# Performance work log

Measured on AMD Instinct MI355X. Metric: run time of the kernel, lower is better.

Reference implementation:

```python
import jax, jax.numpy as jnp
import numpy as np
from jax import lax

NUM_INPUT = 4
NUM_OUTPUT = 1
NUM_U = 10
N = NUM_U // NUM_OUTPUT          # MPC horizon
BATCH = 1024
NINEQ_U = 2 * NUM_U              # input box constraints
NINEQ_X = 2 * NUM_INPUT * N      # soft state constraints
NZ = NUM_U                       # control decision variable dim
NE = NINEQ_X                     # slack variable dim
NW = NZ + NE                     # combined QP variable w = [z; e]
IPM_ITERS = 20                   # fixed-iteration primal-dual interior point
SIGMA = 0.1                      # centering parameter
REG = 1e-8                       # KKT regularization


def setup_inputs():
    key = jax.random.key(0)
    ks = jax.random.split(key, 6)
    x = 0.5 * jax.random.normal(ks[0], (BATCH, NUM_INPUT), dtype=jnp.float32)
    # equality constraint pins z0 = u0; keep inside the |z| <= 0.5 box so QP is feasible
    u0 = (jax.random.uniform(ks[1], (BATCH, NUM_OUTPUT), dtype=jnp.float32) - 0.5) * 0.8
    Q_sqrt = jax.random.uniform(ks[2], (NUM_INPUT, NUM_INPUT), dtype=jnp.float32)
    R_sqrt = jax.random.uniform(ks[3], (NUM_OUTPUT, NUM_OUTPUT), dtype=jnp.float32)
    # scale A so that A^N stays bounded (torch init rand() would blow up at N=10)
    A_dyn = 0.3 * jax.random.uniform(ks[4], (NUM_INPUT, NUM_INPUT), dtype=jnp.float32)
    B_dyn = jax.random.uniform(ks[5], (NUM_INPUT, NUM_OUTPUT), dtype=jnp.float32)
    return {"x": x, "u0": u0, "Q_sqrt": Q_sqrt, "R_sqrt": R_sqrt,
            "A_dyn": A_dyn, "B_dyn": B_dyn}


def _build_mpc_blocks(A, B):
    # A_hat = [A; A^2; ...; A^N],  B_hat = lower block-Toeplitz of A^k B
    Apows = [A]
    for _ in range(1, N):
        Apows.append(Apows[-1] @ A)
    A_hat = jnp.concatenate(Apows, axis=0)                 # (N*n, n)
    T = [B]
    for _ in range(1, N):
        T.append(A @ T[-1])
    T = jnp.stack(T)                                        # (N, n, m), T[k] = A^k B
    i = jnp.arange(N)
    diff = i[:, None] - i[None, :]
    blocks = jnp.where((diff >= 0)[:, :, None, None],
                       T[jnp.clip(diff, 0, N - 1)], 0.0)    # (N, N, n, m)
    B_hat = blocks.transpose(0, 2, 1, 3).reshape(N * NUM_INPUT, N * NUM_OUTPUT)
    return A_hat, B_hat


def _max_step(v, dv):
    # largest alpha keeping v + alpha*dv > 0 (per batch row)
    ratio = jnp.where(dv < -1e-12, -v / jnp.minimum(dv, -1e-12), 1e8)
    return jnp.min(ratio, axis=-1, keepdims=True)


def _qp_solve(H, q, G, h, Aeq, beq):
    # min 0.5 w^T H w + q^T w  s.t. G w <= h, Aeq w = beq
    # H, G, Aeq shared; q, h, beq batched. Infeasible-start primal-dual IPM.
    b, nw = q.shape
    mI = G.shape[0]
    ne = Aeq.shape[0]
    w = jnp.zeros((b, nw), q.dtype)
    nu = jnp.zeros((b, ne), q.dtype)
    s = jnp.maximum(h, 1.0)
    lam = jnp.ones((b, mI), q.dtype)
    I_nw = jnp.eye(nw, dtype=q.dtype)
    I_ne = jnp.eye(ne, dtype=q.dtype)

    def step(carry, _):
        w, s, lam, nu = carry
        Gw = w @ G.T
        r_dual = w @ H + q + lam @ G + nu @ Aeq            # (b, nw)
        r_prim = Gw + s - h                                # (b, mI)
        r_eq = w @ Aeq.T - beq                             # (b, ne)
        mu = SIGMA * jnp.sum(s * lam, axis=-1, keepdims=True) / mI
        d = lam / s
        tmp = (mu - lam * s + lam * r_prim) / s
        rw = -(r_dual + tmp @ G)
        rn = -r_eq
        # Schur complement in w: M = H + G^T diag(lam/s) G
        M = H[None] + (G.T[None, :, :] * d[:, None, :]) @ G + REG * I_nw
        AeqT = jnp.broadcast_to(Aeq.T[None], (b, nw, ne))
        AeqB = jnp.broadcast_to(Aeq[None], (b, ne, nw))
        corner = jnp.broadcast_to((-REG * I_ne)[None], (b, ne, ne))
        K = jnp.concatenate([jnp.concatenate([M, AeqT], axis=2),
                             jnp.concatenate([AeqB, corner], axis=2)], axis=1)
        rhs = jnp.concatenate([rw, rn], axis=1)
        sol = jnp.linalg.solve(K, rhs[..., None])[..., 0]
        dw, dnu = sol[:, :nw], sol[:, nw:]
        ds = -(dw @ G.T) - r_prim
        dlam = (mu - lam * s - lam * ds) / s
        alpha = 0.99 * jnp.minimum(1.0, jnp.minimum(_max_step(s, ds),
                                                    _max_step(lam, dlam)))
        return (w + alpha * dw, s + alpha * ds,
                lam + alpha * dlam, nu + alpha * dnu), None

    (w, s, lam, nu), _ = lax.scan(step, (w, s, lam, nu), None, length=IPM_ITERS)
    return w


def _forward(x, u0, Q_sqrt, R_sqrt, A_dyn, B_dyn):
    b = x.shape[0]
    dt = x.dtype
    x0 = x.reshape(b, -1)
    A_hat, B_hat = _build_mpc_blocks(A_dyn, B_dyn)
    Q = Q_sqrt @ Q_sqrt.T
    R = R_sqrt @ R_sqrt.T
    Q_diag = jnp.kron(jnp.eye(N, dtype=dt), Q)   # block-diag(Q,...,Q,P) with P = Q
    R_diag = jnp.kron(jnp.eye(N, dtype=dt), R)
    Q_hat = B_hat.T @ (Q_diag @ B_hat) + R_diag  # (nz, nz)
    A_x0 = x0 @ A_hat.T                           # (b, n*N)
    p = 2.0 * A_x0 @ (Q_diag @ B_hat)             # (b, nz)
    G1 = jnp.concatenate([jnp.eye(NZ, dtype=dt), -jnp.eye(NZ, dtype=dt)], axis=0)
    G2 = jnp.concatenate([B_hat, -B_hat], axis=0)
    h1 = 0.5 * jnp.ones((b, NINEQ_U), dt)
    h21 = 4.0 * jnp.ones((b, NUM_INPUT * N), dt) - A_x0
    h22 = 4.0 * jnp.ones((b, NUM_INPUT * N), dt) + A_x0
    h2 = jnp.concatenate([h21, h22], axis=1)
    E = jnp.eye(NE, dtype=dt)                     # E_sqrt = I so E = I
    # combined QP over w = [z; e]:
    #   min z^T Q_hat z + p^T z + e^T E e
    #   s.t. G1 z <= h1, G2 z - e <= h2, -e <= 0, F z = f
    # (sum_squares(sqrtm(Q_hat) z) == z^T Q_hat z, so sqrtm cancels exactly)
    H = 2.0 * jnp.block([[Q_hat, jnp.zeros((NZ, NE), dt)],
                         [jnp.zeros((NE, NZ), dt), E]])
    q = jnp.concatenate([p, jnp.zeros((b, NE), dt)], axis=1)
    Ie = jnp.eye(NE, dtype=dt)
    G_all = jnp.concatenate([
        jnp.concatenate([G1, jnp.zeros((NINEQ_U, NE), dt)], axis=1),
        jnp.concatenate([G2, -Ie], axis=1),
        jnp.concatenate([jnp.zeros((NE, NZ), dt), -Ie], axis=1)], axis=0)
    h_all = jnp.concatenate([h1, h2, jnp.zeros((b, NE), dt)], axis=1)
    F = jnp.zeros((1, NW), dt).at[0, 0].set(1.0)  # F z = f with F = e_0^T (padded over e)
    beq = u0.reshape(b, -1)
    w = _qp_solve(H, q, G_all, h_all, F, beq)
    u_opt = w[:, :NZ]
    e_opt = w[:, NZ:]
    a = jnp.sum((u_opt @ Q_hat) * u_opt + p * u_opt, axis=1)
    bterm = jnp.sum((A_x0 @ Q_diag) * A_x0, axis=1)
    c = jnp.sum((x0 @ Q) * x0, axis=1)
    dterm = jnp.sum((e_opt @ E) * e_opt, axis=1)
    cost_opt = (a + bterm + c + dterm)[:, None]
    u0_opt = u_opt[:, 0]   # weight vector is e_0
    return cost_opt, u0_opt


def reference(x, u0, Q_sqrt, R_sqrt, A_dyn, B_dyn):
    return _forward(x, u0, Q_sqrt, R_sqrt, A_dyn, B_dyn)
```

## Files before the change

### kernel.cpp

```cpp
#include <hip/hip_runtime.h>

#define BATCH 1024
#define ITERS 20
#define SIGMA_C 0.1f
#define REG_C 1e-8f

__device__ __forceinline__ float frcp(float x) { return __builtin_amdgcn_rcpf(x); }
__device__ __forceinline__ float readlane_f(float v, int l) {
    return __int_as_float(__builtin_amdgcn_readlane(__float_as_int(v), l));
}
#define DPPF(v, ctrl) \
    __int_as_float(__builtin_amdgcn_update_dpp(0, __float_as_int(v), ctrl, 0xf, 0xf, true))

__device__ __forceinline__ float wave_sum(float v) {
    v += DPPF(v, 0xB1);
    v += DPPF(v, 0x4E);
    v += DPPF(v, 0x141);
    v += DPPF(v, 0x140);
    v += __shfl_xor(v, 16);
    v += __shfl_xor(v, 32);
    return v;
}
__device__ __forceinline__ float wave_min(float v) {
    v = fminf(v, DPPF(v, 0xB1));
    v = fminf(v, DPPF(v, 0x4E));
    v = fminf(v, DPPF(v, 0x141));
    v = fminf(v, DPPF(v, 0x140));
    v = fminf(v, __shfl_xor(v, 16));
    v = fminf(v, __shfl_xor(v, 32));
    return v;
}

__global__ __launch_bounds__(64, 1) void ipm_kernel(
    const float* __restrict__ x, const float* __restrict__ u0p,
    const float* __restrict__ Qs, const float* __restrict__ Rs,
    const float* __restrict__ Ad, const float* __restrict__ Bd,
    float* __restrict__ out)
{
    const int item = blockIdx.x;
    const int lane = threadIdx.x;

    __shared__ __align__(16) float BLc[10 * 40];
    __shared__ __align__(16) float QBc[10 * 40];
    __shared__ __align__(16) float yL4[40];
    __shared__ __align__(16) float QhL[10 * 12];
    __shared__ __align__(16) float SL[10 * 12];
    __shared__ __align__(16) float cg[80];
    __shared__ float duL[20], ltL[20];
    __shared__ float axL[40];
    __shared__ float pvL[10], wL[10];
    __shared__ float QL[16];
    __shared__ float TL[40];
    __shared__ float AhL[160];

    const int r2 = (lane >> 2) & 3, c2 = lane & 3;
    const int r4 = lane & 3;

    if (lane < 16) {
        float acc = 0.f;
        #pragma unroll
        for (int k = 0; k < 4; ++k) acc += Qs[r2 * 4 + k] * Qs[c2 * 4 + k];
        QL[lane] = acc;
    }

    float acol[4];
    #pragma unroll
    for (int k = 0; k < 4; ++k) acol[k] = Ad[k * 4 + c2];
    float cur = Ad[r2 * 4 + c2];
    if (lane < 16) AhL[r2 * 4 + c2] = cur;
    #pragma unroll
    for (int i = 1; i < 10; ++i) {
        float nx = 0.f;
        #pragma unroll
        for (int k = 0; k < 4; ++k) nx += __shfl(cur, r2 * 4 + k) * acol[k];
        cur = nx;
        if (lane < 16) AhL[(4 * i + r2) * 4 + c2] = cur;
    }

    float arow[4];
    #pragma unroll
    for (int k = 0; k < 4; ++k) arow[k] = Ad[r4 * 4 + k];
    float tc = Bd[r4];
    if (lane < 4) TL[r4] = tc;
    #pragma unroll
    for (int i = 1; i < 10; ++i) {
        float nt = 0.f;
        #pragma unroll
        for (int k = 0; k < 4; ++k) nt += arow[k] * __shfl(tc, k);
        tc = nt;
        if (lane < 4) TL[i * 4 + r4] = nt;
    }
    __syncthreads();

    const int kk40 = (lane < 40) ? lane : 39;
    const int ib = lane >> 2;
    float b[10];
    #pragma unroll
    for (int j = 0; j < 10; ++j) {
        int dd = ib - j;
        int dc = dd < 0 ? 0 : (dd > 9 ? 9 : dd);
        float v = TL[dc * 4 + r4];
        b[j] = (dd >= 0 && lane < 40) ? v : 0.f;
    }

    const float xv0 = x[item * 4 + 0], xv1 = x[item * 4 + 1];
    const float xv2 = x[item * 4 + 2], xv3 = x[item * 4 + 3];
    const float ax = AhL[kk40 * 4 + 0] * xv0 + AhL[kk40 * 4 + 1] * xv1 +
                     AhL[kk40 * 4 + 2] * xv2 + AhL[kk40 * 4 + 3] * xv3;
    if (lane < 40) axL[lane] = ax;

    const int gbase = lane & ~3;
    float yv = 0.f;
    #pragma unroll
    for (int rp_ = 0; rp_ < 4; ++rp_) yv += QL[r4 * 4 + rp_] * __shfl(ax, gbase + rp_);
    if (lane < 40) yL4[lane] = yv;
    #pragma unroll
    for (int cc = 0; cc < 10; ++cc) {
        float acc = 0.f;
        #pragma unroll
        for (int rp_ = 0; rp_ < 4; ++rp_) acc += QL[r4 * 4 + rp_] * __shfl(b[cc], gbase + rp_);
        if (lane < 40) QBc[cc * 40 + lane] = acc;
    }
    if (lane < 40) {
        #pragma unroll
        for (int j = 0; j < 10; ++j) BLc[j * 40 + lane] = b[j];
    }
    __syncthreads();

    if (lane < 10) {
        const float4* br = reinterpret_cast<const float4*>(&BLc[lane * 40]);
        const float4* yy = reinterpret_cast<const float4*>(yL4);
        float acc = 0.f;
        #pragma unroll
        for (int i = 0; i < 10; ++i) {
            const float4 a_ = br[i], b_ = yy[i];
            acc += a_.x * b_.x + a_.y * b_.y + a_.z * b_.z + a_.w * b_.w;
        }
        pvL[lane] = 2.f * acc;
    }
    const float R2v = Rs[0] * Rs[0];
    #pragma unroll
    for (int p = 0; p < 2; ++p) {
        const int t = lane + 64 * p;
        if (t < 100) {
            const int aa = t / 10, bb = t - aa * 10;
            const float4* ba = reinterpret_cast<const float4*>(&BLc[aa * 40]);
            const float4* qb = reinterpret_cast<const float4*>(&QBc[bb * 40]);
            float acc = (aa == bb) ? R2v : 0.f;
            #pragma unroll
            for (int i = 0; i < 10; ++i) {
                const float4 a_ = ba[i], b_ = qb[i];
                acc += a_.x * b_.x + a_.y * b_.y + a_.z * b_.z + a_.w * b_.w;
            }
            QhL[aa * 12 + bb] = acc;
        }
    }
    __syncthreads();

    const int t1 = 2 * lane;
    const int srow = t1 / 10, sc1 = t1 - srow * 10, sc2 = sc1 + 1;
    const int rr = lane - 50;
    float tabA[40], tabB[40];
    float qh_a = 0.f, qh_b = 0.f;
    bool diagA = false, diagB = false;
    int drow = 0;
    if (lane < 50) {
        const float4* br = reinterpret_cast<const float4*>(&BLc[srow * 40]);
        const float4* b1 = reinterpret_cast<const float4*>(&BLc[sc1 * 40]);
        const float4* b2 = reinterpret_cast<const float4*>(&BLc[sc2 * 40]);
        #pragma unroll
        for (int i = 0; i < 10; ++i) {
            const float4 r_ = br[i], u_ = b1[i], v_ = b2[i];
            tabA[4*i+0] = r_.x * u_.x; tabA[4*i+1] = r_.y * u_.y;
            tabA[4*i+2] = r_.z * u_.z; tabA[4*i+3] = r_.w * u_.w;
            tabB[4*i+0] = r_.x * v_.x; tabB[4*i+1] = r_.y * v_.y;
            tabB[4*i+2] = r_.z * v_.z; tabB[4*i+3] = r_.w * v_.w;
        }
        qh_a = 2.f * QhL[srow * 12 + sc1];
        qh_b = 2.f * QhL[srow * 12 + sc2];
        diagA = (srow == sc1); diagB = (srow == sc2);
        drow = srow;
    } else if (lane < 60) {
        const float4* br = reinterpret_cast<const float4*>(&BLc[rr * 40]);
        #pragma unroll
        for (int i = 0; i < 10; ++i) {
            const float4 r_ = br[i];
            tabA[4*i+0] = r_.x; tabA[4*i+1] = r_.y;
            tabA[4*i+2] = r_.z; tabA[4*i+3] = r_.w;
        }
        #pragma unroll
        for (int c = 0; c < 10; ++c) tabB[c] = QhL[rr * 12 + c];
        qh_a = pvL[rr];
    }
    __syncthreads();

    float s_B = fmaxf(4.f - ax, 1.f), s_C = fmaxf(4.f + ax, 1.f);
    float s_D = 1.f, s_E = 1.f, s_U = 1.f;
    float l_B = 1.f, l_C = 1.f, l_D = 1.f, l_E = 1.f, l_U = 1.f;
    float w2a = 0.f, w2b = 0.f;
    float w1[10];
    #pragma unroll
    for (int r = 0; r < 10; ++r) w1[r] = 0.f;
    float w1own = 0.f, nu = 0.f;
    const float uu0 = u0p[item];
    const bool a40 = lane < 40, a20 = lane < 20;
    const int jown = (lane < 10) ? lane : lane - 10;
    const float sgnU = (lane < 10) ? 1.f : -1.f;

    for (int it = 0; it < ITERS; ++it) {
        const float rs_B = frcp(s_B), rs_C = frcp(s_C), rs_D = frcp(s_D),
                    rs_E = frcp(s_E), rs_U = frcp(s_U);
        const float d_B = l_B * rs_B, d_C = l_C * rs_C, d_D = l_D * rs_D,
                    d_E = l_E * rs_E, d_U = l_U * rs_U;
        float part = a40 ? (s_B * l_B + s_C * l_C + s_D * l_D + s_E * l_E) : 0.f;
        if (a20) part += s_U * l_U;
        const float mu = SIGMA_C * wave_sum(part) * (1.f / 180.f);

        float Bu = 0.f;
        #pragma unroll
        for (int j = 0; j < 10; ++j) Bu += b[j] * w1[j];

        const float rp_B = Bu - w2a + s_B - (4.f - ax);
        const float rp_C = -Bu - w2b + s_C - (4.f + ax);
        const float rp_D = -w2a + s_D;
        const float rp_E = -w2b + s_E;
        const float rp_U = sgnU * w1own + s_U - 0.5f;

        const float tm_B = (mu - l_B * s_B + l_B * rp_B) * rs_B;
        const float tm_C = (mu - l_C * s_C + l_C * rp_C) * rs_C;
        const float tm_D = (mu - l_D * s_D + l_D * rp_D) * rs_D;
        const float tm_E = (mu - l_E * s_E + l_E * rp_E) * rs_E;
        const float tm_U = (mu - l_U * s_U + l_U * rp_U) * rs_U;
        const float lt_B = l_B + tm_B, lt_C = l_C + tm_C, lt_D = l_D + tm_D,
                    lt_E = l_E + tm_E;

        const float D22a = 2.f + d_B + d_D + REG_C, D22b = 2.f + d_C + d_E + REG_C;
        const float rda = frcp(D22a), rdb = frcp(D22b);
        const float rw2a = -2.f * w2a + lt_B + lt_D;
        const float rw2b = -2.f * w2b + lt_C + lt_E;
        const float coeff = (d_B + d_C) - d_B * d_B * rda - d_C * d_C * rdb;
        const float gvc = (d_B * rw2a * rda - d_C * rw2b * rdb) - (lt_B - lt_C);

        if (a40) { cg[lane] = coeff; cg[40 + lane] = gvc; }
        if (a20) { duL[lane] = d_U; ltL[lane] = l_U + tm_U; }
        __syncthreads();

        float4 cf[10];
        {
            const float4* cp = reinterpret_cast<const float4*>(cg + ((lane >= 50) ? 40 : 0));
            #pragma unroll
            for (int i = 0; i < 10; ++i) cf[i] = cp[i];
        }
        if (lane < 50) {
            float accA = 0.f, accB = 0.f;
            #pragma unroll
            for (int i = 0; i < 10; ++i) {
                accA += tabA[4*i+0]*cf[i].x + tabA[4*i+1]*cf[i].y +
                        tabA[4*i+2]*cf[i].z + tabA[4*i+3]*cf[i].w;
                accB += tabB[4*i+0]*cf[i].x + tabB[4*i+1]*cf[i].y +
                        tabB[4*i+2]*cf[i].z + tabB[4*i+3]*cf[i].w;
            }
            float vA = accA + qh_a, vB = accB + qh_b;
            if (diagA || diagB) {
                const float dd = duL[drow] + duL[10 + drow] + REG_C;
                if (diagA) vA += dd; else vB += dd;
            }
            *reinterpret_cast<float2*>(&SL[srow * 12 + sc1]) = make_float2(vA, vB);
        } else if (lane < 60) {
            float acc = 0.f;
            #pragma unroll
            for (int i = 0; i < 10; ++i)
                acc += tabA[4*i+0]*cf[i].x + tabA[4*i+1]*cf[i].y +
                       tabA[4*i+2]*cf[i].z + tabA[4*i+3]*cf[i].w;
            float qw = 0.f;
            #pragma unroll
            for (int c = 0; c < 10; ++c) qw += tabB[c] * w1[c];
            SL[rr * 12 + 10] =
                acc - (2.f * qw + qh_a + ltL[rr] - ltL[10 + rr] + ((rr == 0) ? nu : 0.f));
        }
        __syncthreads();

        float row[11], rBv;
        if (lane < 10) {
            const float4* s4 = reinterpret_cast<const float4*>(&SL[lane * 12]);
            const float4 q0 = s4[0], q1 = s4[1], q2 = s4[2];
            row[0] = q0.x; row[1] = q0.y; row[2] = q0.z; row[3] = q0.w;
            row[4] = q1.x; row[5] = q1.y; row[6] = q1.z; row[7] = q1.w;
            row[8] = q2.x; row[9] = q2.y; row[10] = q2.z;
        } else {
            #pragma unroll
            for (int c = 0; c < 11; ++c) row[c] = 0.f;
        }
        rBv = (lane == 0) ? 1.f : 0.f;

        #pragma unroll
        for (int kc = 0; kc < 9; ++kc) {
            float pk[11];
            #pragma unroll
            for (int c = kc; c < 11; ++c) pk[c] = readlane_f(row[c], kc);
            const float pB = readlane_f(rBv, kc);
            const float rpiv = frcp(pk[kc]);
            const float f = (lane > kc) ? row[kc] * rpiv : 0.f;
            #pragma unroll
            for (int c = kc + 1; c < 11; ++c) row[c] -= f * pk[c];
            rBv -= f * pB;
        }

        float rd[10];
        #pragma unroll
        for (int r = 0; r < 10; ++r) rd[r] = frcp(row[r]);

        float dwAv[10], dwBv[10], ownA = 0.f, ownB = 0.f;
        #pragma unroll
        for (int r = 9; r >= 0; --r) {
            const float bA = readlane_f(row[10] * rd[r], r);
            const float bB = readlane_f(rBv * rd[r], r);
            dwAv[r] = bA; dwBv[r] = bB;
            if (jown == r) { ownA = bA; ownB = bB; }
            const float m_ = (lane < r) ? 1.f : 0.f;
            row[10] -= m_ * row[r] * bA;
            rBv     -= m_ * row[r] * bB;
        }

        const float rn = -(w1[0] - uu0);
        const float nu_d = (dwAv[0] - rn) * frcp(dwBv[0] + REG_C);
        float dw1[10];
        #pragma unroll
        for (int r = 0; r < 10; ++r) dw1[r] = dwAv[r] - nu_d * dwBv[r];
        const float dOwn = ownA - nu_d * ownB;

        float Bdw = 0.f;
        #pragma unroll
        for (int j = 0; j < 10; ++j) Bdw += b[j] * dw1[j];
        const float dw2a = (rw2a + d_B * Bdw) * rda;
        const float dw2b = (rw2b - d_C * Bdw) * rdb;

        const float ds_B = -(Bdw - dw2a) - rp_B;
        const float ds_C = (Bdw + dw2b) - rp_C;
        const float ds_D = dw2a - rp_D;
        const float ds_E = dw2b - rp_E;
        const float ds_U = -sgnU * dOwn - rp_U;
        const float dl_B = (mu - l_B * s_B - l_B * ds_B) * rs_B;
        const float dl_C = (mu - l_C * s_C - l_C * ds_C) * rs_C;
        const float dl_D = (mu - l_D * s_D - l_D * ds_D) * rs_D;
        const float dl_E = (mu - l_E * s_E - l_E * ds_E) * rs_E;
        const float dl_U = (mu - l_U * s_U - l_U * ds_U) * rs_U;

        float rmin = 1.f;
        if (a40) {
            if (ds_B < -1e-12f) rmin = fminf(rmin, -s_B * frcp(ds_B));
            if (ds_C < -1e-12f) rmin = fminf(rmin, -s_C * frcp(ds_C));
            if (ds_D < -1e-12f) rmin = fminf(rmin, -s_D * frcp(ds_D));
            if (ds_E < -1e-12f) rmin = fminf(rmin, -s_E * frcp(ds_E));
            if (dl_B < -1e-12f) rmin = fminf(rmin, -l_B * frcp(dl_B));
            if (dl_C < -1e-12f) rmin = fminf(rmin, -l_C * frcp(dl_C));
            if (dl_D < -1e-12f) rmin = fminf(rmin, -l_D * frcp(dl_D));
            if (dl_E < -1e-12f) rmin = fminf(rmin, -l_E * frcp(dl_E));
        }
        if (a20) {
            if (ds_U < -1e-12f) rmin = fminf(rmin, -s_U * frcp(ds_U));
            if (dl_U < -1e-12f) rmin = fminf(rmin, -l_U * frcp(dl_U));
        }
        const float alpha = 0.99f * wave_min(rmin);

        s_B += alpha * ds_B; s_C += alpha * ds_C; s_D += alpha * ds_D;
        s_E += alpha * ds_E; s_U += alpha * ds_U;
        l_B += alpha * dl_B; l_C += alpha * dl_C; l_D += alpha * dl_D;
        l_E += alpha * dl_E; l_U += alpha * dl_U;
        w2a += alpha * dw2a; w2b += alpha * dw2b;
        #pragma unroll
        for (int r = 0; r < 10; ++r) w1[r] += alpha * dw1[r];
        w1own += alpha * dOwn;
        nu += alpha * nu_d;
    }

    if (lane == 0) {
        #pragma unroll
        for (int r = 0; r < 10; ++r) wL[r] = w1[r];
    }
    __syncthreads();
    float part = a40 ? (w2a * w2a + w2b * w2b) : 0.f;
    for (int idx = lane; idx < 100; idx += 64) {
        const int r = idx / 10, c = idx - r * 10;
        part += wL[r] * QhL[r * 12 + c] * wL[c];
    }
    if (lane < 10) part += pvL[lane] * wL[lane];
    for (int idx = lane; idx < 160; idx += 64) {
        const int i2 = idx >> 4, rc = idx & 15, rr2 = rc >> 2, cc2 = rc & 3;
        part += axL[i2 * 4 + rr2] * QL[rc] * axL[i2 * 4 + cc2];
    }
    if (lane == 0) {
        float ct = 0.f;
        #pragma unroll
        for (int r = 0; r < 4; ++r) {
            const float xr = (r == 0 ? xv0 : r == 1 ? xv1 : r == 2 ? xv2 : xv3);
            #pragma unroll
            for (int c = 0; c < 4; ++c) {
                const float xc = (c == 0 ? xv0 : c == 1 ? xv1 : c == 2 ? xv2 : xv3);
                ct += xr * QL[r * 4 + c] * xc;
            }
        }
        part += ct;
    }
    const float cost = wave_sum(part);
    if (lane == 0) {
        out[item] = cost;
        out[BATCH + item] = w1[0];
    }
}

extern "C" void kernel_launch(void* const* d_in, const int* in_sizes, int n_in,
                              void* d_out, int out_size, void* d_ws, size_t ws_size,
                              hipStream_t stream) {
    const float* x  = (const float*)d_in[0];
    const float* u0 = (const float*)d_in[1];
    const float* Qs = (const float*)d_in[2];
    const float* Rs = (const float*)d_in[3];
    const float* Ad = (const float*)d_in[4];
    const float* Bd = (const float*)d_in[5];
    float* outp = (float*)d_out;
    ipm_kernel<<<dim3(BATCH), dim3(64), 0, stream>>>(x, u0, Qs, Rs, Ad, Bd, outp);
}
```

Baseline: 101.4 us.

## Use 2x2 block Gauss-Jordan elimination and fuse mu reduction into step reduction

Replaces the per-column elimination and back-substitution of the 10x10 KKT solve with 2x2 pivot-block Gauss-Jordan steps, halving the number of serial readlane broadcast rounds. The duality-gap reduction for the next iteration's mu is folded into the alpha min-reduction: the next mu is computed as a quadratic in alpha from three partial sums, so the same DPP passes serve both reductions. This removes one full wave reduction per iteration and shortens the serial dependency chain. The cost is extra arithmetic, unpivoted 2x2 block inverses that may be less numerically robust, and an s*l product evaluated in a different order.

```diff
diff --git a/kernel.cpp b/kernel.cpp
--- a/kernel.cpp
+++ b/kernel.cpp
@@ -21,15 +21,13 @@
     v += __shfl_xor(v, 32);
     return v;
 }
-__device__ __forceinline__ float wave_min(float v) {
-    v = fminf(v, DPPF(v, 0xB1));
-    v = fminf(v, DPPF(v, 0x4E));
-    v = fminf(v, DPPF(v, 0x141));
-    v = fminf(v, DPPF(v, 0x140));
-    v = fminf(v, __shfl_xor(v, 16));
-    v = fminf(v, __shfl_xor(v, 32));
-    return v;
-}
+
+#define RED4_DPP(ctrl) do { \
+    p0 += DPPF(p0, ctrl); \
+    p1 += DPPF(p1, ctrl); \
+    p2 += DPPF(p2, ctrl); \
+    rmin = fminf(rmin, DPPF(rmin, ctrl)); \
+} while (0)
 
 __global__ __launch_bounds__(64, 1) void ipm_kernel(
     const float* __restrict__ x, const float* __restrict__ u0p,
@@ -207,14 +205,18 @@
     const int jown = (lane < 10) ? lane : lane - 10;
     const float sgnU = (lane < 10) ? 1.f : -1.f;
 
+    float mu;
+    {
+        float part = a40 ? (s_B * l_B + s_C * l_C + s_D * l_D + s_E * l_E) : 0.f;
+        if (a20) part += s_U * l_U;
+        mu = SIGMA_C * wave_sum(part) * (1.f / 180.f);
+    }
+
     for (int it = 0; it < ITERS; ++it) {
         const float rs_B = frcp(s_B), rs_C = frcp(s_C), rs_D = frcp(s_D),
                     rs_E = frcp(s_E), rs_U = frcp(s_U);
         const float d_B = l_B * rs_B, d_C = l_C * rs_C, d_D = l_D * rs_D,
                     d_E = l_E * rs_E, d_U = l_U * rs_U;
-        float part = a40 ? (s_B * l_B + s_C * l_C + s_D * l_D + s_E * l_E) : 0.f;
-        if (a20) part += s_U * l_U;
-        const float mu = SIGMA_C * wave_sum(part) * (1.f / 180.f);
 
         float Bu = 0.f;
         #pragma unroll
@@ -280,7 +282,7 @@
         }
         __syncthreads();
 
-        float row[11], rBv;
+        float row[12];
         if (lane < 10) {
             const float4* s4 = reinterpret_cast<const float4*>(&SL[lane * 12]);
             const float4 q0 = s4[0], q1 = s4[1], q2 = s4[2];
@@ -291,43 +293,54 @@
             #pragma unroll
             for (int c = 0; c < 11; ++c) row[c] = 0.f;
         }
-        rBv = (lane == 0) ? 1.f : 0.f;
-
-        #pragma unroll
-        for (int kc = 0; kc < 9; ++kc) {
-            float pk[11];
-            #pragma unroll
-            for (int c = kc; c < 11; ++c) pk[c] = readlane_f(row[c], kc);
-            const float pB = readlane_f(rBv, kc);
-            const float rpiv = frcp(pk[kc]);
-            const float f = (lane > kc) ? row[kc] * rpiv : 0.f;
-            #pragma unroll
-            for (int c = kc + 1; c < 11; ++c) row[c] -= f * pk[c];
-            rBv -= f * pB;
-        }
-
-        float rd[10];
-        #pragma unroll
-        for (int r = 0; r < 10; ++r) rd[r] = frcp(row[r]);
-
-        float dwAv[10], dwBv[10], ownA = 0.f, ownB = 0.f;
-        #pragma unroll
-        for (int r = 9; r >= 0; --r) {
-            const float bA = readlane_f(row[10] * rd[r], r);
-            const float bB = readlane_f(rBv * rd[r], r);
-            dwAv[r] = bA; dwBv[r] = bB;
-            if (jown == r) { ownA = bA; ownB = bB; }
-            const float m_ = (lane < r) ? 1.f : 0.f;
-            row[10] -= m_ * row[r] * bA;
-            rBv     -= m_ * row[r] * bB;
+        row[11] = (lane == 0) ? 1.f : 0.f;
+
+        #pragma unroll
+        for (int kb = 0; kb < 5; ++kb) {
+            const int bb = 2 * kb;
+            float pA[12], pB[12];
+            #pragma unroll
+            for (int c = 0; c < 12; ++c) {
+                if (c >= bb) {
+                    pA[c] = readlane_f(row[c], bb);
+                    pB[c] = readlane_f(row[c], bb + 1);
+                }
+            }
+            const float rdet = frcp(pA[bb] * pB[bb + 1] - pA[bb + 1] * pB[bb]);
+            const bool act = (lane < 10) && (lane != bb) && (lane != bb + 1);
+            const float f1 = act ? (row[bb] * pB[bb + 1] - row[bb + 1] * pB[bb]) * rdet : 0.f;
+            const float f2 = act ? (row[bb + 1] * pA[bb] - row[bb] * pA[bb + 1]) * rdet : 0.f;
+            #pragma unroll
+            for (int c = 0; c < 12; ++c) {
+                if (c >= bb + 2) row[c] -= f1 * pA[c] + f2 * pB[c];
+            }
+        }
+
+        float xA[10], xB[10];
+        #pragma unroll
+        for (int kb = 0; kb < 5; ++kb) {
+            const int bb = 2 * kb;
+            const float a_  = readlane_f(row[bb],     bb);
+            const float b_  = readlane_f(row[bb + 1], bb);
+            const float c_  = readlane_f(row[bb],     bb + 1);
+            const float d_  = readlane_f(row[bb + 1], bb + 1);
+            const float rA0 = readlane_f(row[10], bb),     rB0 = readlane_f(row[11], bb);
+            const float rA1 = readlane_f(row[10], bb + 1), rB1 = readlane_f(row[11], bb + 1);
+            const float rdet = frcp(a_ * d_ - b_ * c_);
+            xA[bb]     = (d_ * rA0 - b_ * rA1) * rdet;
+            xA[bb + 1] = (a_ * rA1 - c_ * rA0) * rdet;
+            xB[bb]     = (d_ * rB0 - b_ * rB1) * rdet;
+            xB[bb + 1] = (a_ * rB1 - c_ * rB0) * rdet;
         }
 
         const float rn = -(w1[0] - uu0);
-        const float nu_d = (dwAv[0] - rn) * frcp(dwBv[0] + REG_C);
+        const float nu_d = (xA[0] - rn) * frcp(xB[0] + REG_C);
         float dw1[10];
         #pragma unroll
-        for (int r = 0; r < 10; ++r) dw1[r] = dwAv[r] - nu_d * dwBv[r];
-        const float dOwn = ownA - nu_d * ownB;
+        for (int r = 0; r < 10; ++r) dw1[r] = xA[r] - nu_d * xB[r];
+        float dOwn = 0.f;
+        #pragma unroll
+        for (int r = 0; r < 10; ++r) dOwn = (jown == r) ? dw1[r] : dOwn;
 
         float Bdw = 0.f;
         #pragma unroll
@@ -346,7 +359,7 @@
         const float dl_E = (mu - l_E * s_E - l_E * ds_E) * rs_E;
         const float dl_U = (mu - l_U * s_U - l_U * ds_U) * rs_U;
 
-        float rmin = 1.f;
+        float rmin = 1.f, p0 = 0.f, p1 = 0.f, p2 = 0.f;
         if (a40) {
             if (ds_B < -1e-12f) rmin = fminf(rmin, -s_B * frcp(ds_B));
             if (ds_C < -1e-12f) rmin = fminf(rmin, -s_C * frcp(ds_C));
@@ -356,12 +369,29 @@
             if (dl_C < -1e-12f) rmin = fminf(rmin, -l_C * frcp(dl_C));
             if (dl_D < -1e-12f) rmin = fminf(rmin, -l_D * frcp(dl_D));
             if (dl_E < -1e-12f) rmin = fminf(rmin, -l_E * frcp(dl_E));
+            p0 = s_B * l_B + s_C * l_C + s_D * l_D + s_E * l_E;
+            p1 = (s_B * dl_B + l_B * ds_B) + (s_C * dl_C + l_C * ds_C) +
+                 (s_D * dl_D + l_D * ds_D) + (s_E * dl_E + l_E * ds_E);
+            p2 = ds_B * dl_B + ds_C * dl_C + ds_D * dl_D + ds_E * dl_E;
         }
         if (a20) {
             if (ds_U < -1e-12f) rmin = fminf(rmin, -s_U * frcp(ds_U));
             if (dl_U < -1e-12f) rmin = fminf(rmin, -l_U * frcp(dl_U));
-        }
-        const float alpha = 0.99f * wave_min(rmin);
+            p0 += s_U * l_U;
+            p1 += s_U * dl_U + l_U * ds_U;
+            p2 += ds_U * dl_U;
+        }
+        RED4_DPP(0xB1);
+        RED4_DPP(0x4E);
+        RED4_DPP(0x141);
+        RED4_DPP(0x140);
+        p0 += __shfl_xor(p0, 16); p1 += __shfl_xor(p1, 16); p2 += __shfl_xor(p2, 16);
+        rmin = fminf(rmin, __shfl_xor(rmin, 16));
+        p0 += __shfl_xor(p0, 32); p1 += __shfl_xor(p1, 32); p2 += __shfl_xor(p2, 32);
+        rmin = fminf(rmin, __shfl_xor(rmin, 32));
+
+        const float alpha = 0.99f * rmin;
+        mu = SIGMA_C * (p0 + alpha * (p1 + alpha * p2)) * (1.f / 180.f);
 
         s_B += alpha * ds_B; s_C += alpha * ds_C; s_D += alpha * ds_D;
         s_E += alpha * ds_E; s_U += alpha * ds_U;
```

Result: no change. 101.3 us (-0.1%).

## Carry next-iteration mu algebraically and fuse reductions with step-length min

Applied to the files above, without the earlier changes.

The barrier parameter for the next iteration is computed in closed form as p0 + alpha*p1 + alpha^2*p2. The three terms are reduced in the same DPP/shuffle sequence as the step-length minimum, which takes the dependent wave_sum for mu off the start of each iteration. Dot products are split into several independent accumulators to shorten dependency chains. B*dw is now built from precomputed B*dwA and B*dwB, so it no longer waits on nu_d. Rounding can differ slightly from recomputing mu directly.

```diff
diff --git a/kernel.cpp b/kernel.cpp
--- a/kernel.cpp
+++ b/kernel.cpp
@@ -21,15 +21,12 @@
     v += __shfl_xor(v, 32);
     return v;
 }
-__device__ __forceinline__ float wave_min(float v) {
-    v = fminf(v, DPPF(v, 0xB1));
-    v = fminf(v, DPPF(v, 0x4E));
-    v = fminf(v, DPPF(v, 0x141));
-    v = fminf(v, DPPF(v, 0x140));
-    v = fminf(v, __shfl_xor(v, 16));
-    v = fminf(v, __shfl_xor(v, 32));
-    return v;
-}
+
+#define RED3_DPP(ctrl) do { \
+    p1 += DPPF(p1, ctrl); \
+    p2 += DPPF(p2, ctrl); \
+    rmin = fminf(rmin, DPPF(rmin, ctrl)); \
+} while (0)
 
 __global__ __launch_bounds__(64, 1) void ipm_kernel(
     const float* __restrict__ x, const float* __restrict__ u0p,
@@ -207,18 +204,29 @@
     const int jown = (lane < 10) ? lane : lane - 10;
     const float sgnU = (lane < 10) ? 1.f : -1.f;
 
+    float mu;
+    {
+        float part = a40 ? (s_B * l_B + s_C * l_C + s_D * l_D + s_E * l_E) : 0.f;
+        if (a20) part += s_U * l_U;
+        mu = SIGMA_C * wave_sum(part) * (1.f / 180.f);
+    }
+
     for (int it = 0; it < ITERS; ++it) {
         const float rs_B = frcp(s_B), rs_C = frcp(s_C), rs_D = frcp(s_D),
                     rs_E = frcp(s_E), rs_U = frcp(s_U);
         const float d_B = l_B * rs_B, d_C = l_C * rs_C, d_D = l_D * rs_D,
                     d_E = l_E * rs_E, d_U = l_U * rs_U;
-        float part = a40 ? (s_B * l_B + s_C * l_C + s_D * l_D + s_E * l_E) : 0.f;
-        if (a20) part += s_U * l_U;
-        const float mu = SIGMA_C * wave_sum(part) * (1.f / 180.f);
-
-        float Bu = 0.f;
-        #pragma unroll
-        for (int j = 0; j < 10; ++j) Bu += b[j] * w1[j];
+
+        float p0 = a40 ? (s_B * l_B + s_C * l_C + s_D * l_D + s_E * l_E) : 0.f;
+        if (a20) p0 += s_U * l_U;
+        p0 = wave_sum(p0);
+
+        float Bu0 = 0.f, Bu1 = 0.f;
+        #pragma unroll
+        for (int j = 0; j < 5; ++j) Bu0 += b[j] * w1[j];
+        #pragma unroll
+        for (int j = 5; j < 10; ++j) Bu1 += b[j] * w1[j];
+        const float Bu = Bu0 + Bu1;
 
         const float rp_B = Bu - w2a + s_B - (4.f - ax);
         const float rp_C = -Bu - w2b + s_C - (4.f + ax);
@@ -252,29 +260,36 @@
             for (int i = 0; i < 10; ++i) cf[i] = cp[i];
         }
         if (lane < 50) {
-            float accA = 0.f, accB = 0.f;
+            float aA0 = 0.f, aA1 = 0.f, aA2 = 0.f, aA3 = 0.f;
+            float aB0 = 0.f, aB1 = 0.f, aB2 = 0.f, aB3 = 0.f;
             #pragma unroll
             for (int i = 0; i < 10; ++i) {
-                accA += tabA[4*i+0]*cf[i].x + tabA[4*i+1]*cf[i].y +
-                        tabA[4*i+2]*cf[i].z + tabA[4*i+3]*cf[i].w;
-                accB += tabB[4*i+0]*cf[i].x + tabB[4*i+1]*cf[i].y +
-                        tabB[4*i+2]*cf[i].z + tabB[4*i+3]*cf[i].w;
+                aA0 += tabA[4*i+0] * cf[i].x; aA1 += tabA[4*i+1] * cf[i].y;
+                aA2 += tabA[4*i+2] * cf[i].z; aA3 += tabA[4*i+3] * cf[i].w;
+                aB0 += tabB[4*i+0] * cf[i].x; aB1 += tabB[4*i+1] * cf[i].y;
+                aB2 += tabB[4*i+2] * cf[i].z; aB3 += tabB[4*i+3] * cf[i].w;
             }
-            float vA = accA + qh_a, vB = accB + qh_b;
+            float vA = ((aA0 + aA1) + (aA2 + aA3)) + qh_a;
+            float vB = ((aB0 + aB1) + (aB2 + aB3)) + qh_b;
             if (diagA || diagB) {
                 const float dd = duL[drow] + duL[10 + drow] + REG_C;
                 if (diagA) vA += dd; else vB += dd;
             }
             *reinterpret_cast<float2*>(&SL[srow * 12 + sc1]) = make_float2(vA, vB);
         } else if (lane < 60) {
-            float acc = 0.f;
-            #pragma unroll
-            for (int i = 0; i < 10; ++i)
-                acc += tabA[4*i+0]*cf[i].x + tabA[4*i+1]*cf[i].y +
-                       tabA[4*i+2]*cf[i].z + tabA[4*i+3]*cf[i].w;
-            float qw = 0.f;
-            #pragma unroll
-            for (int c = 0; c < 10; ++c) qw += tabB[c] * w1[c];
+            float a0 = 0.f, a1 = 0.f, a2 = 0.f, a3 = 0.f;
+            #pragma unroll
+            for (int i = 0; i < 10; ++i) {
+                a0 += tabA[4*i+0] * cf[i].x; a1 += tabA[4*i+1] * cf[i].y;
+                a2 += tabA[4*i+2] * cf[i].z; a3 += tabA[4*i+3] * cf[i].w;
+            }
+            const float acc = (a0 + a1) + (a2 + a3);
+            float qw0 = 0.f, qw1 = 0.f;
+            #pragma unroll
+            for (int c = 0; c < 5; ++c) qw0 += tabB[c] * w1[c];
+            #pragma unroll
+            for (int c = 5; c < 10; ++c) qw1 += tabB[c] * w1[c];
+            const float qw = qw0 + qw1;
             SL[rr * 12 + 10] =
                 acc - (2.f * qw + qh_a + ltL[rr] - ltL[10 + rr] + ((rr == 0) ? nu : 0.f));
         }
@@ -322,16 +337,21 @@
             rBv     -= m_ * row[r] * bB;
         }
 
+        float bA0 = 0.f, bA1 = 0.f, bB0 = 0.f, bB1 = 0.f;
+        #pragma unroll
+        for (int j = 0; j < 5; ++j) { bA0 += b[j] * dwAv[j]; bB0 += b[j] * dwBv[j]; }
+        #pragma unroll
+        for (int j = 5; j < 10; ++j) { bA1 += b[j] * dwAv[j]; bB1 += b[j] * dwBv[j]; }
+        const float BdwA = bA0 + bA1, BdwB = bB0 + bB1;
+
         const float rn = -(w1[0] - uu0);
         const float nu_d = (dwAv[0] - rn) * frcp(dwBv[0] + REG_C);
         float dw1[10];
         #pragma unroll
         for (int r = 0; r < 10; ++r) dw1[r] = dwAv[r] - nu_d * dwBv[r];
         const float dOwn = ownA - nu_d * ownB;
-
-        float Bdw = 0.f;
-        #pragma unroll
-        for (int j = 0; j < 10; ++j) Bdw += b[j] * dw1[j];
+        const float Bdw = BdwA - nu_d * BdwB;
+
         const float dw2a = (rw2a + d_B * Bdw) * rda;
         const float dw2b = (rw2b - d_C * Bdw) * rdb;
 
@@ -346,7 +366,7 @@
         const float dl_E = (mu - l_E * s_E - l_E * ds_E) * rs_E;
         const float dl_U = (mu - l_U * s_U - l_U * ds_U) * rs_U;
 
-        float rmin = 1.f;
+        float rmin = 1.f, p1 = 0.f, p2 = 0.f;
         if (a40) {
             if (ds_B < -1e-12f) rmin = fminf(rmin, -s_B * frcp(ds_B));
             if (ds_C < -1e-12f) rmin = fminf(rmin, -s_C * frcp(ds_C));
@@ -356,12 +376,27 @@
             if (dl_C < -1e-12f) rmin = fminf(rmin, -l_C * frcp(dl_C));
             if (dl_D < -1e-12f) rmin = fminf(rmin, -l_D * frcp(dl_D));
             if (dl_E < -1e-12f) rmin = fminf(rmin, -l_E * frcp(dl_E));
+            p1 = (s_B * dl_B + l_B * ds_B) + (s_C * dl_C + l_C * ds_C) +
+                 (s_D * dl_D + l_D * ds_D) + (s_E * dl_E + l_E * ds_E);
+            p2 = ds_B * dl_B + ds_C * dl_C + ds_D * dl_D + ds_E * dl_E;
         }
         if (a20) {
             if (ds_U < -1e-12f) rmin = fminf(rmin, -s_U * frcp(ds_U));
             if (dl_U < -1e-12f) rmin = fminf(rmin, -l_U * frcp(dl_U));
-        }
-        const float alpha = 0.99f * wave_min(rmin);
+            p1 += s_U * dl_U + l_U * ds_U;
+            p2 += ds_U * dl_U;
+        }
+        RED3_DPP(0xB1);
+        RED3_DPP(0x4E);
+        RED3_DPP(0x141);
+        RED3_DPP(0x140);
+        p1 += __shfl_xor(p1, 16); p2 += __shfl_xor(p2, 16);
+        rmin = fminf(rmin, __shfl_xor(rmin, 16));
+        p1 += __shfl_xor(p1, 32); p2 += __shfl_xor(p2, 32);
+        rmin = fminf(rmin, __shfl_xor(rmin, 32));
+
+        const float alpha = 0.99f * rmin;
+        mu = SIGMA_C * (p0 + alpha * (p1 + alpha * p2)) * (1.f / 180.f);
 
         s_B += alpha * ds_B; s_C += alpha * ds_C; s_D += alpha * ds_D;
         s_E += alpha * ds_E; s_U += alpha * ds_U;
```

Result: no change. 102.7 us (+1.3%).

## Fuse step-length and next-mu reductions, packed FMA dot products

Applied to the files above, without the earlier changes.

Rewrites the step-length search as a max of -d/v ratios, using reciprocals of s and l instead of one division per component. The next iteration's mu comes from a quadratic in alpha (p0 + alpha*p1 + alpha^2*p2), so mu and alpha now share a single batched DPP/shuffle reduction instead of two separate wave reductions per iteration. The small dot products are also recast as packed two-wide float FMAs. This shortens the serial per-iteration reduction chain at the cost of extra reciprocals and slightly different rounding.

```diff
diff --git a/kernel.cpp b/kernel.cpp
--- a/kernel.cpp
+++ b/kernel.cpp
@@ -5,10 +5,15 @@
 #define SIGMA_C 0.1f
 #define REG_C 1e-8f
 
+typedef float f2 __attribute__((ext_vector_type(2)));
+
 __device__ __forceinline__ float frcp(float x) { return __builtin_amdgcn_rcpf(x); }
 __device__ __forceinline__ float readlane_f(float v, int l) {
     return __int_as_float(__builtin_amdgcn_readlane(__float_as_int(v), l));
 }
+__device__ __forceinline__ f2 mkf2(float a, float b) { f2 r; r.x = a; r.y = b; return r; }
+__device__ __forceinline__ f2 fma2(f2 a, f2 b, f2 c) { return a * b + c; }
+
 #define DPPF(v, ctrl) \
     __int_as_float(__builtin_amdgcn_update_dpp(0, __float_as_int(v), ctrl, 0xf, 0xf, true))
 
@@ -21,15 +26,13 @@
     v += __shfl_xor(v, 32);
     return v;
 }
-__device__ __forceinline__ float wave_min(float v) {
-    v = fminf(v, DPPF(v, 0xB1));
-    v = fminf(v, DPPF(v, 0x4E));
-    v = fminf(v, DPPF(v, 0x141));
-    v = fminf(v, DPPF(v, 0x140));
-    v = fminf(v, __shfl_xor(v, 16));
-    v = fminf(v, __shfl_xor(v, 32));
-    return v;
-}
+
+#define RED4_DPP(ctrl) do { \
+    p0 += DPPF(p0, ctrl); \
+    p1 += DPPF(p1, ctrl); \
+    p2 += DPPF(p2, ctrl); \
+    q = fmaxf(q, DPPF(q, ctrl)); \
+} while (0)
 
 __global__ __launch_bounds__(64, 1) void ipm_kernel(
     const float* __restrict__ x, const float* __restrict__ u0p,
@@ -160,7 +163,7 @@
     const int t1 = 2 * lane;
     const int srow = t1 / 10, sc1 = t1 - srow * 10, sc2 = sc1 + 1;
     const int rr = lane - 50;
-    float tabA[40], tabB[40];
+    f2 tA[20], tB[20];
     float qh_a = 0.f, qh_b = 0.f;
     bool diagA = false, diagB = false;
     int drow = 0;
@@ -171,10 +174,10 @@
         #pragma unroll
         for (int i = 0; i < 10; ++i) {
             const float4 r_ = br[i], u_ = b1[i], v_ = b2[i];
-            tabA[4*i+0] = r_.x * u_.x; tabA[4*i+1] = r_.y * u_.y;
-            tabA[4*i+2] = r_.z * u_.z; tabA[4*i+3] = r_.w * u_.w;
-            tabB[4*i+0] = r_.x * v_.x; tabB[4*i+1] = r_.y * v_.y;
-            tabB[4*i+2] = r_.z * v_.z; tabB[4*i+3] = r_.w * v_.w;
+            tA[2*i]   = mkf2(r_.x * u_.x, r_.y * u_.y);
+            tA[2*i+1] = mkf2(r_.z * u_.z, r_.w * u_.w);
+            tB[2*i]   = mkf2(r_.x * v_.x, r_.y * v_.y);
+            tB[2*i+1] = mkf2(r_.z * v_.z, r_.w * v_.w);
         }
         qh_a = 2.f * QhL[srow * 12 + sc1];
         qh_b = 2.f * QhL[srow * 12 + sc2];
@@ -185,11 +188,12 @@
         #pragma unroll
         for (int i = 0; i < 10; ++i) {
             const float4 r_ = br[i];
-            tabA[4*i+0] = r_.x; tabA[4*i+1] = r_.y;
-            tabA[4*i+2] = r_.z; tabA[4*i+3] = r_.w;
-        }
-        #pragma unroll
-        for (int c = 0; c < 10; ++c) tabB[c] = QhL[rr * 12 + c];
+            tA[2*i]   = mkf2(r_.x, r_.y);
+            tA[2*i+1] = mkf2(r_.z, r_.w);
+        }
+        #pragma unroll
+        for (int c = 0; c < 5; ++c)
+            tB[c] = mkf2(QhL[rr * 12 + 2*c], QhL[rr * 12 + 2*c + 1]);
         qh_a = pvL[rr];
     }
     __syncthreads();
@@ -207,18 +211,26 @@
     const int jown = (lane < 10) ? lane : lane - 10;
     const float sgnU = (lane < 10) ? 1.f : -1.f;
 
+    float mu;
+    {
+        float part = a40 ? (s_B * l_B + s_C * l_C + s_D * l_D + s_E * l_E) : 0.f;
+        if (a20) part += s_U * l_U;
+        mu = SIGMA_C * wave_sum(part) * (1.f / 180.f);
+    }
+
     for (int it = 0; it < ITERS; ++it) {
         const float rs_B = frcp(s_B), rs_C = frcp(s_C), rs_D = frcp(s_D),
                     rs_E = frcp(s_E), rs_U = frcp(s_U);
+        const float rl_B = frcp(l_B), rl_C = frcp(l_C), rl_D = frcp(l_D),
+                    rl_E = frcp(l_E), rl_U = frcp(l_U);
         const float d_B = l_B * rs_B, d_C = l_C * rs_C, d_D = l_D * rs_D,
                     d_E = l_E * rs_E, d_U = l_U * rs_U;
-        float part = a40 ? (s_B * l_B + s_C * l_C + s_D * l_D + s_E * l_E) : 0.f;
-        if (a20) part += s_U * l_U;
-        const float mu = SIGMA_C * wave_sum(part) * (1.f / 180.f);
-
-        float Bu = 0.f;
-        #pragma unroll
-        for (int j = 0; j < 10; ++j) Bu += b[j] * w1[j];
+
+        f2 bu = mkf2(0.f, 0.f);
+        #pragma unroll
+        for (int j = 0; j < 5; ++j)
+            bu = fma2(mkf2(b[2*j], b[2*j+1]), mkf2(w1[2*j], w1[2*j+1]), bu);
+        const float Bu = bu.x + bu.y;
 
         const float rp_B = Bu - w2a + s_B - (4.f - ax);
         const float rp_C = -Bu - w2b + s_C - (4.f + ax);
@@ -245,36 +257,43 @@
         if (a20) { duL[lane] = d_U; ltL[lane] = l_U + tm_U; }
         __syncthreads();
 
-        float4 cf[10];
+        float4 cf4[10];
         {
             const float4* cp = reinterpret_cast<const float4*>(cg + ((lane >= 50) ? 40 : 0));
             #pragma unroll
-            for (int i = 0; i < 10; ++i) cf[i] = cp[i];
+            for (int i = 0; i < 10; ++i) cf4[i] = cp[i];
         }
         if (lane < 50) {
-            float accA = 0.f, accB = 0.f;
+            f2 aA0 = mkf2(0.f, 0.f), aA1 = mkf2(0.f, 0.f);
+            f2 aB0 = mkf2(0.f, 0.f), aB1 = mkf2(0.f, 0.f);
             #pragma unroll
             for (int i = 0; i < 10; ++i) {
-                accA += tabA[4*i+0]*cf[i].x + tabA[4*i+1]*cf[i].y +
-                        tabA[4*i+2]*cf[i].z + tabA[4*i+3]*cf[i].w;
-                accB += tabB[4*i+0]*cf[i].x + tabB[4*i+1]*cf[i].y +
-                        tabB[4*i+2]*cf[i].z + tabB[4*i+3]*cf[i].w;
+                const f2 cl = mkf2(cf4[i].x, cf4[i].y);
+                const f2 ch = mkf2(cf4[i].z, cf4[i].w);
+                aA0 = fma2(tA[2*i], cl, aA0); aA1 = fma2(tA[2*i+1], ch, aA1);
+                aB0 = fma2(tB[2*i], cl, aB0); aB1 = fma2(tB[2*i+1], ch, aB1);
             }
-            float vA = accA + qh_a, vB = accB + qh_b;
+            float vA = ((aA0.x + aA0.y) + (aA1.x + aA1.y)) + qh_a;
+            float vB = ((aB0.x + aB0.y) + (aB1.x + aB1.y)) + qh_b;
             if (diagA || diagB) {
                 const float dd = duL[drow] + duL[10 + drow] + REG_C;
                 if (diagA) vA += dd; else vB += dd;
             }
             *reinterpret_cast<float2*>(&SL[srow * 12 + sc1]) = make_float2(vA, vB);
         } else if (lane < 60) {
-            float acc = 0.f;
-            #pragma unroll
-            for (int i = 0; i < 10; ++i)
-                acc += tabA[4*i+0]*cf[i].x + tabA[4*i+1]*cf[i].y +
-                       tabA[4*i+2]*cf[i].z + tabA[4*i+3]*cf[i].w;
-            float qw = 0.f;
-            #pragma unroll
-            for (int c = 0; c < 10; ++c) qw += tabB[c] * w1[c];
+            f2 a0 = mkf2(0.f, 0.f), a1 = mkf2(0.f, 0.f);
+            #pragma unroll
+            for (int i = 0; i < 10; ++i) {
+                const f2 cl = mkf2(cf4[i].x, cf4[i].y);
+                const f2 ch = mkf2(cf4[i].z, cf4[i].w);
+                a0 = fma2(tA[2*i], cl, a0); a1 = fma2(tA[2*i+1], ch, a1);
+            }
+            const float acc = (a0.x + a0.y) + (a1.x + a1.y);
+            f2 qa = mkf2(0.f, 0.f);
+            #pragma unroll
+            for (int c = 0; c < 5; ++c)
+                qa = fma2(tB[c], mkf2(w1[2*c], w1[2*c+1]), qa);
+            const float qw = qa.x + qa.y;
             SL[rr * 12 + 10] =
                 acc - (2.f * qw + qh_a + ltL[rr] - ltL[10 + rr] + ((rr == 0) ? nu : 0.f));
         }
@@ -329,9 +348,12 @@
         for (int r = 0; r < 10; ++r) dw1[r] = dwAv[r] - nu_d * dwBv[r];
         const float dOwn = ownA - nu_d * ownB;
 
-        float Bdw = 0.f;
-        #pragma unroll
-        for (int j = 0; j < 10; ++j) Bdw += b[j] * dw1[j];
+        f2 bd = mkf2(0.f, 0.f);
+        #pragma unroll
+        for (int j = 0; j < 5; ++j)
+            bd = fma2(mkf2(b[2*j], b[2*j+1]), mkf2(dw1[2*j], dw1[2*j+1]), bd);
+        const float Bdw = bd.x + bd.y;
+
         const float dw2a = (rw2a + d_B * Bdw) * rda;
         const float dw2b = (rw2b - d_C * Bdw) * rdb;
 
@@ -346,22 +368,39 @@
         const float dl_E = (mu - l_E * s_E - l_E * ds_E) * rs_E;
         const float dl_U = (mu - l_U * s_U - l_U * ds_U) * rs_U;
 
-        float rmin = 1.f;
+        float q = 0.f, p0 = 0.f, p1 = 0.f, p2 = 0.f;
         if (a40) {
-            if (ds_B < -1e-12f) rmin = fminf(rmin, -s_B * frcp(ds_B));
-            if (ds_C < -1e-12f) rmin = fminf(rmin, -s_C * frcp(ds_C));
-            if (ds_D < -1e-12f) rmin = fminf(rmin, -s_D * frcp(ds_D));
-            if (ds_E < -1e-12f) rmin = fminf(rmin, -s_E * frcp(ds_E));
-            if (dl_B < -1e-12f) rmin = fminf(rmin, -l_B * frcp(dl_B));
-            if (dl_C < -1e-12f) rmin = fminf(rmin, -l_C * frcp(dl_C));
-            if (dl_D < -1e-12f) rmin = fminf(rmin, -l_D * frcp(dl_D));
-            if (dl_E < -1e-12f) rmin = fminf(rmin, -l_E * frcp(dl_E));
+            q = fmaxf(q, (ds_B < -1e-12f) ? -ds_B * rs_B : 0.f);
+            q = fmaxf(q, (ds_C < -1e-12f) ? -ds_C * rs_C : 0.f);
+            q = fmaxf(q, (ds_D < -1e-12f) ? -ds_D * rs_D : 0.f);
+            q = fmaxf(q, (ds_E < -1e-12f) ? -ds_E * rs_E : 0.f);
+            q = fmaxf(q, (dl_B < -1e-12f) ? -dl_B * rl_B : 0.f);
+            q = fmaxf(q, (dl_C < -1e-12f) ? -dl_C * rl_C : 0.f);
+            q = fmaxf(q, (dl_D < -1e-12f) ? -dl_D * rl_D : 0.f);
+            q = fmaxf(q, (dl_E < -1e-12f) ? -dl_E * rl_E : 0.f);
+            p0 = s_B * l_B + s_C * l_C + s_D * l_D + s_E * l_E;
+            p1 = (s_B * dl_B + l_B * ds_B) + (s_C * dl_C + l_C * ds_C) +
+                 (s_D * dl_D + l_D * ds_D) + (s_E * dl_E + l_E * ds_E);
+            p2 = ds_B * dl_B + ds_C * dl_C + ds_D * dl_D + ds_E * dl_E;
         }
         if (a20) {
-            if (ds_U < -1e-12f) rmin = fminf(rmin, -s_U * frcp(ds_U));
-            if (dl_U < -1e-12f) rmin = fminf(rmin, -l_U * frcp(dl_U));
-        }
-        const float alpha = 0.99f * wave_min(rmin);
+            q = fmaxf(q, (ds_U < -1e-12f) ? -ds_U * rs_U : 0.f);
+            q = fmaxf(q, (dl_U < -1e-12f) ? -dl_U * rl_U : 0.f);
+            p0 += s_U * l_U;
+            p1 += s_U * dl_U + l_U * ds_U;
+            p2 += ds_U * dl_U;
+        }
+        RED4_DPP(0xB1);
+        RED4_DPP(0x4E);
+        RED4_DPP(0x141);
+        RED4_DPP(0x140);
+        p0 += __shfl_xor(p0, 16); p1 += __shfl_xor(p1, 16); p2 += __shfl_xor(p2, 16);
+        q = fmaxf(q, __shfl_xor(q, 16));
+        p0 += __shfl_xor(p0, 32); p1 += __shfl_xor(p1, 32); p2 += __shfl_xor(p2, 32);
+        q = fmaxf(q, __shfl_xor(q, 32));
+
+        const float alpha = 0.99f * ((q > 1.f) ? frcp(q) : 1.f);
+        mu = SIGMA_C * (p0 + alpha * (p1 + alpha * p2)) * (1.f / 180.f);
 
         s_B += alpha * ds_B; s_C += alpha * ds_C; s_D += alpha * ds_D;
         s_E += alpha * ds_E; s_U += alpha * ds_U;
```

New measurement: 99.50 us. No clear change (-1.9%).
